# Optimization experiments

Measured on AMD Instinct MI355X. Metric: run time of the kernel, lower is better.

Reference implementation:

```python
import jax, jax.numpy as jnp
import numpy as np


def setup_inputs() -> dict:
    key = jax.random.key(0)
    k1, k2, k3, k4 = jax.random.split(key, 4)
    vocab, dim, batch, neg_size = 1000000, 128, 16384, 20
    return {
        "target_input": jax.random.randint(k1, (batch,), 0, vocab),
        "context": jax.random.randint(k2, (batch,), 0, vocab),
        "neg": jax.random.randint(k3, (batch, neg_size), 0, vocab),
        "emb": jax.random.normal(k4, (vocab, dim), dtype=jnp.float32),
    }


def reference(target_input, context, neg, emb):
    v = emb[target_input]            # [B, D]
    u = emb[context]                 # [B, D]
    pos = jax.nn.log_sigmoid(jnp.sum(u * v, axis=1))           # [B]
    u_hat = emb[neg]                 # [B, K, D]
    neg_scores = jnp.einsum("bkd,bd->bk", u_hat, v)             # [B, K]
    neg_val = jax.nn.log_sigmoid(-jnp.sum(neg_scores, axis=1))  # [B]
    return -jnp.mean(pos + neg_val)
```

## Files before the change

kernel.cpp:

```cpp
#include <hip/hip_runtime.h>
#include <math.h>

#define DIM 128
#define NEG_K 20

__device__ __forceinline__ float log_sigmoid(float x) {
    float m = fminf(x, 0.0f);
    return m - log1pf(__expf(-fabsf(x)));
}

__global__ __launch_bounds__(256) void sgns_partial_kernel(
    const int* __restrict__ target,
    const int* __restrict__ context,
    const int* __restrict__ neg,
    const float* __restrict__ emb,
    float* __restrict__ partials,
    int B)
{
    const int lane = threadIdx.x & 63;
    const int wid  = __builtin_amdgcn_readfirstlane(
                         (blockIdx.x * blockDim.x + threadIdx.x) >> 6);
    const int nW   = (gridDim.x * blockDim.x) >> 6;

    float local = 0.0f;
    for (int b = wid; b < B; b += nW) {
        const int tgt = __builtin_amdgcn_readfirstlane(target[b]);
        const int ctx = __builtin_amdgcn_readfirstlane(context[b]);

        int ni[NEG_K];
        const int* __restrict__ nb = neg + (size_t)b * NEG_K;
        #pragma unroll
        for (int k = 0; k < NEG_K; ++k)
            ni[k] = __builtin_amdgcn_readfirstlane(nb[k]);

        const float2 v = ((const float2*)(emb + (size_t)tgt * DIM))[lane];
        const float2 u = ((const float2*)(emb + (size_t)ctx * DIM))[lane];

        float2 ns = make_float2(0.f, 0.f);
        #pragma unroll
        for (int k = 0; k < NEG_K; ++k) {
            const float2 un = ((const float2*)(emb + (size_t)ni[k] * DIM))[lane];
            ns.x += un.x; ns.y += un.y;
        }

        float pos = u.x * v.x + u.y * v.y;
        float ng  = ns.x * v.x + ns.y * v.y;

        #pragma unroll
        for (int off = 32; off; off >>= 1) {
            pos += __shfl_xor(pos, off);
            ng  += __shfl_xor(ng,  off);
        }
        if (lane == 0) local += log_sigmoid(pos) + log_sigmoid(-ng);
    }

    __shared__ float wsum[4];
    if (lane == 0) wsum[threadIdx.x >> 6] = local;
    __syncthreads();
    if (threadIdx.x == 0)
        partials[blockIdx.x] = wsum[0] + wsum[1] + wsum[2] + wsum[3];
}

__global__ __launch_bounds__(256) void sgns_reduce_kernel(
    const float* __restrict__ partials, float* __restrict__ out,
    int n, float invB)
{
    float s = 0.0f;
    for (int i = threadIdx.x; i < n; i += 256) s += partials[i];
    #pragma unroll
    for (int off = 32; off; off >>= 1) s += __shfl_xor(s, off);

    __shared__ float wsum[4];
    const int lane = threadIdx.x & 63;
    if (lane == 0) wsum[threadIdx.x >> 6] = s;
    __syncthreads();
    if (threadIdx.x == 0)
        out[0] = -(wsum[0] + wsum[1] + wsum[2] + wsum[3]) * invB;
}

extern "C" void kernel_launch(void* const* d_in, const int* in_sizes, int n_in,
                              void* d_out, int out_size, void* d_ws, size_t ws_size,
                              hipStream_t stream) {
    const int*   target  = (const int*)d_in[0];
    const int*   context = (const int*)d_in[1];
    const int*   neg     = (const int*)d_in[2];
    const float* emb     = (const float*)d_in[3];
    float* out      = (float*)d_out;
    float* partials = (float*)d_ws;
    const int B = in_sizes[0];

    const int threads = 256;
    const int blocks  = (B + 3) / 4;

    sgns_partial_kernel<<<blocks, threads, 0, stream>>>(target, context, neg,
                                                        emb, partials, B);
    sgns_reduce_kernel<<<1, threads, 0, stream>>>(partials, out, blocks,
                                                  1.0f / (float)B);
}
```

Baseline: 587.0 us.

## Bucket-sort embedding row lookups by row index to improve gather locality

Replaces the per-sample gather kernel with a multi-kernel pipeline. It histograms and counting-sorts all context and negative row lookups into buckets by row index, then computes each dot product against a pre-gathered target buffer and reduces per-sample results. The intent is to make the random 512-byte row reads from the large embedding table more sequential and cache-friendly. In exchange it adds eight kernel launches, global atomics, and extra global traffic for the task list, the target buffer and the per-task results. Separate per-negative dots are also summed instead of summing the negative vectors first.

```diff
diff --git a/kernel.cpp b/kernel.cpp
--- a/kernel.cpp
+++ b/kernel.cpp
@@ -3,59 +3,124 @@
 
 #define DIM 128
 #define NEG_K 20
+#define NBUCKET 4096
+
+typedef unsigned int u32;
+typedef unsigned long long u64;
 
 __device__ __forceinline__ float log_sigmoid(float x) {
     float m = fminf(x, 0.0f);
     return m - log1pf(__expf(-fabsf(x)));
 }
 
-__global__ __launch_bounds__(256) void sgns_partial_kernel(
-    const int* __restrict__ target,
-    const int* __restrict__ context,
-    const int* __restrict__ neg,
-    const float* __restrict__ emb,
-    float* __restrict__ partials,
-    int B)
-{
+
+__global__ __launch_bounds__(256) void k_zero_hist(u32* __restrict__ hist) {
+    const int i = blockIdx.x * 256 + threadIdx.x;
+    if (i < NBUCKET) hist[i] = 0u;
+}
+
+__global__ __launch_bounds__(256) void k_vgather(const int* __restrict__ target,
+                                                 const float* __restrict__ emb,
+                                                 float* __restrict__ vbuf, int B) {
     const int lane = threadIdx.x & 63;
-    const int wid  = __builtin_amdgcn_readfirstlane(
-                         (blockIdx.x * blockDim.x + threadIdx.x) >> 6);
-    const int nW   = (gridDim.x * blockDim.x) >> 6;
+    const int b = (blockIdx.x * 256 + threadIdx.x) >> 6;
+    if (b >= B) return;
+    const int tgt = __builtin_amdgcn_readfirstlane(target[b]);
+    ((float2*)(vbuf + (size_t)b * DIM))[lane] =
+        ((const float2*)(emb + (size_t)tgt * DIM))[lane];
+}
 
-    float local = 0.0f;
-    for (int b = wid; b < B; b += nW) {
-        const int tgt = __builtin_amdgcn_readfirstlane(target[b]);
-        const int ctx = __builtin_amdgcn_readfirstlane(context[b]);
+__device__ __forceinline__ u32 task_row(const int* context, const int* neg,
+                                        int b, int k) {
+    return (u32)((k < NEG_K) ? neg[b * NEG_K + k] : context[b]);
+}
 
-        int ni[NEG_K];
-        const int* __restrict__ nb = neg + (size_t)b * NEG_K;
+__global__ __launch_bounds__(256) void k_hist(const int* __restrict__ context,
+                                              const int* __restrict__ neg,
+                                              u32* __restrict__ hist, int B) {
+    const int t = blockIdx.x * 256 + threadIdx.x;
+    if (t >= B * 21) return;
+    const int b = t / 21, k = t - b * 21;
+    const u32 row = task_row(context, neg, b, k);
+    atomicAdd(&hist[(row >> 8) & (NBUCKET - 1)], 1u);
+}
+
+__global__ __launch_bounds__(256) void k_scan(const u32* __restrict__ hist,
+                                              u32* __restrict__ offs) {
+    __shared__ u32 s[256];
+    const int t = threadIdx.x;
+    u32 loc[16];
+    u32 sum = 0;
+    #pragma unroll
+    for (int i = 0; i < 16; ++i) { loc[i] = hist[t * 16 + i]; sum += loc[i]; }
+    s[t] = sum;
+    __syncthreads();
+    for (int off = 1; off < 256; off <<= 1) {
+        const u32 v = (t >= off) ? s[t - off] : 0u;
+        __syncthreads();
+        s[t] += v;
+        __syncthreads();
+    }
+    u32 run = s[t] - sum;
+    #pragma unroll
+    for (int i = 0; i < 16; ++i) { offs[t * 16 + i] = run; run += loc[i]; }
+}
+
+__global__ __launch_bounds__(256) void k_scatter(const int* __restrict__ context,
+                                                 const int* __restrict__ neg,
+                                                 u32* __restrict__ offs,
+                                                 u64* __restrict__ tasks, int B) {
+    const int t = blockIdx.x * 256 + threadIdx.x;
+    if (t >= B * 21) return;
+    const int b = t / 21, k = t - b * 21;
+    const u32 row = task_row(context, neg, b, k);
+    const u32 p = atomicAdd(&offs[(row >> 8) & (NBUCKET - 1)], 1u);
+    tasks[p] = ((u64)row << 32) | ((u32)b << 5) | (u32)k;
+}
+
+#define TPW 8
+__global__ __launch_bounds__(256) void k_dots(const u64* __restrict__ tasks,
+                                              const float* __restrict__ emb,
+                                              const float* __restrict__ vbuf,
+                                              float* __restrict__ res,
+                                              int B, int NT) {
+    const int lane = threadIdx.x & 63;
+    int base = ((blockIdx.x * 256 + threadIdx.x) >> 6) * TPW;
+    base = __builtin_amdgcn_readfirstlane(base);
+    #pragma unroll
+    for (int i = 0; i < TPW; ++i) {
+        const int ti = base + i;
+        if (ti < NT) {
+            const u64 tv = tasks[ti];
+            const u32 row = (u32)(tv >> 32);
+            const u32 bk  = (u32)tv;
+            const u32 b = bk >> 5, k = bk & 31u;
+            const float2 e  = ((const float2*)(emb  + (size_t)row * DIM))[lane];
+            const float2 vv = ((const float2*)(vbuf + (size_t)b   * DIM))[lane];
+            float d = e.x * vv.x + e.y * vv.y;
+            #pragma unroll
+            for (int off = 32; off; off >>= 1) d += __shfl_xor(d, off);
+            if (lane == 0) res[(int)k * B + (int)b] = d;
+        }
+    }
+}
+
+__global__ __launch_bounds__(256) void k_loss(const float* __restrict__ res,
+                                              float* __restrict__ partials,
+                                              int B) {
+    const int b = blockIdx.x * 256 + threadIdx.x;
+    float term = 0.0f;
+    if (b < B) {
+        float ng = 0.0f;
         #pragma unroll
-        for (int k = 0; k < NEG_K; ++k)
-            ni[k] = __builtin_amdgcn_readfirstlane(nb[k]);
-
-        const float2 v = ((const float2*)(emb + (size_t)tgt * DIM))[lane];
-        const float2 u = ((const float2*)(emb + (size_t)ctx * DIM))[lane];
-
-        float2 ns = make_float2(0.f, 0.f);
-        #pragma unroll
-        for (int k = 0; k < NEG_K; ++k) {
-            const float2 un = ((const float2*)(emb + (size_t)ni[k] * DIM))[lane];
-            ns.x += un.x; ns.y += un.y;
-        }
-
-        float pos = u.x * v.x + u.y * v.y;
-        float ng  = ns.x * v.x + ns.y * v.y;
-
-        #pragma unroll
-        for (int off = 32; off; off >>= 1) {
-            pos += __shfl_xor(pos, off);
-            ng  += __shfl_xor(ng,  off);
-        }
-        if (lane == 0) local += log_sigmoid(pos) + log_sigmoid(-ng);
+        for (int k = 0; k < NEG_K; ++k) ng += res[k * B + b];
+        const float pos = res[NEG_K * B + b];
+        term = log_sigmoid(pos) + log_sigmoid(-ng);
     }
-
+    #pragma unroll
+    for (int off = 32; off; off >>= 1) term += __shfl_xor(term, off);
     __shared__ float wsum[4];
-    if (lane == 0) wsum[threadIdx.x >> 6] = local;
+    if ((threadIdx.x & 63) == 0) wsum[threadIdx.x >> 6] = term;
     __syncthreads();
     if (threadIdx.x == 0)
         partials[blockIdx.x] = wsum[0] + wsum[1] + wsum[2] + wsum[3];
@@ -85,15 +150,33 @@
     const int*   context = (const int*)d_in[1];
     const int*   neg     = (const int*)d_in[2];
     const float* emb     = (const float*)d_in[3];
-    float* out      = (float*)d_out;
-    float* partials = (float*)d_ws;
-    const int B = in_sizes[0];
+    float* out = (float*)d_out;
+    const int B  = in_sizes[0];
+    const int NT = B * 21;
 
-    const int threads = 256;
-    const int blocks  = (B + 3) / 4;
+    char* ws = (char*)d_ws;
+    float* partials = (float*)(ws + 0);
+    u32*   hist     = (u32*)(ws + 16384);
+    u32*   offs     = (u32*)(ws + 32768);
+    size_t off_tasks = 65536;
+    size_t off_res   = (off_tasks + (size_t)NT * 8 + 255) & ~(size_t)255;
+    size_t off_vbuf  = (off_res + (size_t)(NEG_K + 1) * B * 4 + 255) & ~(size_t)255;
+    u64*   tasks = (u64*)(ws + off_tasks);
+    float* res   = (float*)(ws + off_res);
+    float* vbuf  = (float*)(ws + off_vbuf);
 
-    sgns_partial_kernel<<<blocks, threads, 0, stream>>>(target, context, neg,
-                                                        emb, partials, B);
-    sgns_reduce_kernel<<<1, threads, 0, stream>>>(partials, out, blocks,
-                                                  1.0f / (float)B);
+    k_zero_hist<<<(NBUCKET + 255) / 256, 256, 0, stream>>>(hist);
+    k_vgather<<<((size_t)B * 64 + 255) / 256, 256, 0, stream>>>(target, emb, vbuf, B);
+    k_hist<<<(NT + 255) / 256, 256, 0, stream>>>(context, neg, hist, B);
+    k_scan<<<1, 256, 0, stream>>>(hist, offs);
+    k_scatter<<<(NT + 255) / 256, 256, 0, stream>>>(context, neg, offs, tasks, B);
+
+    const int nwaves = (NT + TPW - 1) / TPW;
+    k_dots<<<((size_t)nwaves * 64 + 255) / 256, 256, 0, stream>>>(
+        tasks, emb, vbuf, res, B, NT);
+
+    const int lblocks = (B + 255) / 256;
+    k_loss<<<lblocks, 256, 0, stream>>>(res, partials, B);
+    sgns_reduce_kernel<<<1, 256, 0, stream>>>(partials, out, lblocks,
+                                              1.0f / (float)B);
 }
```

Measured after the change: 659.2 us. +12.3%, slower.
